# Kernel tuning notes

Hardware: AMD Instinct MI355X
Metric: run time of the kernel (lower is better)

The kernel has to match this reference:

```python
import jax, jax.numpy as jnp
import numpy as np

NUM_CLASSES = 81
SCORE_THRESH = 0.05
BBOX_XFORM_CLIP = float(np.log(1000.0 / 16.0))
WX, WY, WW, WH = 10.0, 10.0, 5.0, 5.0           # post-processor box_coder weights


def setup_inputs() -> dict:
    key = jax.random.key(0)
    ks = jax.random.split(key, 10)
    R, C, P, H = 2000, 256, 7, 1024
    D = C * P * P  # 12544
    x = jax.random.normal(ks[0], (R, C, P, P), jnp.float32)
    xy = jax.random.uniform(ks[1], (R, 2), jnp.float32) * 600.0
    wh = jax.random.uniform(ks[2], (R, 2), jnp.float32) * 200.0 + 1.0
    boxes = jnp.concatenate([xy, xy + wh], axis=1)  # valid xyxy proposals
    s = 0.01
    W6 = jax.random.normal(ks[3], (D, H), jnp.float32) * s
    b6 = jnp.zeros((H,), jnp.float32)
    W7 = jax.random.normal(ks[4], (H, H), jnp.float32) * s
    b7 = jnp.zeros((H,), jnp.float32)
    Wcls = jax.random.normal(ks[5], (H, NUM_CLASSES), jnp.float32) * s
    bcls = jnp.zeros((NUM_CLASSES,), jnp.float32)
    Wbox = jax.random.normal(ks[6], (H, NUM_CLASSES * 4), jnp.float32) * s
    bbox_b = jnp.zeros((NUM_CLASSES * 4,), jnp.float32)
    return {"x": x, "boxes": boxes, "W6": W6, "b6": b6, "W7": W7, "b7": b7,
            "Wcls": Wcls, "bcls": bcls, "Wbox": Wbox, "bbox_b": bbox_b}


def _decode(reg, boxes):
    w = boxes[:, 2] - boxes[:, 0] + 1.0
    h = boxes[:, 3] - boxes[:, 1] + 1.0
    cx = boxes[:, 0] + 0.5 * w
    cy = boxes[:, 1] + 0.5 * h
    dx = reg[..., 0] / WX
    dy = reg[..., 1] / WY
    dw = jnp.minimum(reg[..., 2] / WW, BBOX_XFORM_CLIP)
    dh = jnp.minimum(reg[..., 3] / WH, BBOX_XFORM_CLIP)
    pcx = dx * w[:, None] + cx[:, None]
    pcy = dy * h[:, None] + cy[:, None]
    pw = jnp.exp(dw) * w[:, None]
    ph = jnp.exp(dh) * h[:, None]
    return jnp.stack([pcx - 0.5 * pw, pcy - 0.5 * ph,
                      pcx + 0.5 * pw - 1.0, pcy + 0.5 * ph - 1.0], axis=-1)


def reference(x, boxes, W6, b6, W7, b7, Wcls, bcls, Wbox, bbox_b):
    R = x.shape[0]
    f = x.reshape(R, -1)                          # [R, 12544]
    f6 = jax.nn.relu(f @ W6 + b6)                 # roi_output, [R, 1024]
    f7 = jax.nn.relu(f6 @ W7 + b7)                # [R, 1024]
    probs = jax.nn.softmax(f7 @ Wcls + bcls, axis=-1)       # [R, 81]
    reg = (f7 @ Wbox + bbox_b).reshape(R, NUM_CLASSES, 4)   # [R, 81, 4]
    dec = _decode(reg, boxes)                     # [R, 81, 4]
    # per_class_extend, fixed-shape: drop background class 0, mask below threshold
    pj = probs[:, 1:]                             # [R, 80]
    bj = dec[:, 1:, :]                            # [R, 80, 4]
    keep = pj > SCORE_THRESH
    scores_m = jnp.where(keep, pj, 0.0)
    boxes_m = jnp.where(keep[..., None], bj, 0.0).reshape(R, -1)  # [R, 320]
    return jnp.concatenate([scores_m, boxes_m, f6], axis=-1)      # [R, 1424]
```

## Files before the change

kernel.cpp:

```cpp
#include <hip/hip_runtime.h>
#include <stdint.h>

typedef float f32x4 __attribute__((ext_vector_type(4)));
typedef __bf16 bf16x8 __attribute__((ext_vector_type(8)));
typedef unsigned short us4 __attribute__((ext_vector_type(4)));

__device__ __forceinline__ unsigned short f32_to_bf16(float f) {
  union { float f; uint32_t u; } v; v.f = f;
  return (unsigned short)((v.u + 0x7FFFu + ((v.u >> 16) & 1u)) >> 16);
}

__device__ __forceinline__ void gload16(const void* g, void* l) {
  __builtin_amdgcn_global_load_lds((const __attribute__((address_space(1))) void*)g,
                                   (__attribute__((address_space(3))) void*)l, 16, 0, 0);
}

template <int EPI>
__global__ __launch_bounds__(256, 2) void gemm_bf16(
    const unsigned short* __restrict__ A, const unsigned short* __restrict__ Bt,
    int M, int NB, int K, int Mtiles, int Ntiles, int splits,
    float* __restrict__ outF, unsigned short* __restrict__ outH,
    const float* __restrict__ bias, const float* __restrict__ bias2,
    int NV, size_t splitStride)
{
  __shared__ unsigned short lds[16384];
  const int tid = threadIdx.x;
  const int lane = tid & 63;
  const int wave = tid >> 6;

  int bid = blockIdx.x;
  const int mt = bid % Mtiles; bid /= Mtiles;
  const int nt = bid % Ntiles; bid /= Ntiles;
  const int sp = bid;

  const int nK = K >> 5;
  const int chunk = nK / splits;
  const int kBegin = sp * chunk;
  const int kEnd = kBegin + chunk;

  const int rowl = tid & 127;
  const int k8l = tid >> 7;
  int aRow = mt * 128 + rowl; if (aRow > M - 1) aRow = M - 1;
  int bRow = nt * 128 + rowl; if (bRow > NB - 1) bRow = NB - 1;
  const unsigned short* gA = A + (size_t)aRow * K + k8l * 8;
  const unsigned short* gB = Bt + (size_t)bRow * K + k8l * 8;

  const int k8 = lane >> 4;
  const int rsel = lane & 15;
  const int wrBase = (wave >> 1) * 64;
  const int wcBase = (wave & 1) * 64;
  int aOff[4], bOff[4];
#pragma unroll
  for (int m = 0; m < 4; ++m) aOff[m] = (k8 * 128 + wrBase + m * 16 + rsel) * 8;
#pragma unroll
  for (int n = 0; n < 4; ++n) bOff[n] = 4096 + (k8 * 128 + wcBase + n * 16 + rsel) * 8;

  f32x4 acc[4][4];
  const f32x4 zero = {0.f, 0.f, 0.f, 0.f};
#pragma unroll
  for (int m = 0; m < 4; ++m)
#pragma unroll
    for (int n = 0; n < 4; ++n) acc[m][n] = zero;

  auto stage = [&](int kt, int b) {
    const unsigned short* a = gA + kt * 32;
    const unsigned short* bsrc = gB + kt * 32;
    unsigned short* base = &lds[b * 8192];
    gload16(a,         base + tid * 8);
    gload16(a + 16,    base + (tid + 256) * 8);
    gload16(bsrc,      base + 4096 + tid * 8);
    gload16(bsrc + 16, base + 4096 + (tid + 256) * 8);
  };

  stage(kBegin, 0);
  __syncthreads();
  int cur = 0;
  for (int kt = kBegin; kt < kEnd; ++kt) {
    if (kt + 1 < kEnd) stage(kt + 1, cur ^ 1);
    const int cbase = cur * 8192;
    bf16x8 af[4], bfv[4];
#pragma unroll
    for (int m = 0; m < 4; ++m) af[m] = *(const bf16x8*)&lds[cbase + aOff[m]];
#pragma unroll
    for (int n = 0; n < 4; ++n) bfv[n] = *(const bf16x8*)&lds[cbase + bOff[n]];
#pragma unroll
    for (int m = 0; m < 4; ++m)
#pragma unroll
      for (int n = 0; n < 4; ++n)
        acc[m][n] = __builtin_amdgcn_mfma_f32_16x16x32_bf16(af[m], bfv[n], acc[m][n], 0, 0, 0);
    __syncthreads();
    cur ^= 1;
  }

  const int colBase = nt * 128 + wcBase + rsel;
  const int rowBase = mt * 128 + wrBase + (lane >> 4) * 4;
#pragma unroll
  for (int m = 0; m < 4; ++m) {
#pragma unroll
    for (int n = 0; n < 4; ++n) {
      const int col = colBase + n * 16;
#pragma unroll
      for (int j = 0; j < 4; ++j) {
        const int row = rowBase + m * 16 + j;
        if (row < M) {
          float v = acc[m][n][j];
          if (EPI == 0) {
            outF[sp * splitStride + (size_t)row * 1024 + col] = v;
          } else if (EPI == 1) {
            v += bias[col];
            v = fmaxf(v, 0.f);
            outH[(size_t)row * 1024 + col] = f32_to_bf16(v);
          } else {
            if (col < NV) {
              v += (col < 81) ? bias[col] : bias2[col - 81];
              outF[(size_t)row * NV + col] = v;
            }
          }
        }
      }
    }
  }
}

__global__ void transpose_to_bf16(const float* __restrict__ src, unsigned short* __restrict__ dst,
                                  int R, int C, int dstRowOff, int dstLd) {
  __shared__ unsigned short tile[64][66];
  const int c0 = blockIdx.x * 64, r0 = blockIdx.y * 64;
  const int t = threadIdx.x;
  const bool fast = ((C & 3) == 0) && (c0 + 64 <= C);
  const int lr0 = t >> 4;
  const int lc4 = (t & 15) * 4;
#pragma unroll
  for (int i = 0; i < 4; ++i) {
    const int lr = lr0 + i * 16;
    const size_t rowOff = (size_t)(r0 + lr) * C;
    if (fast) {
      f32x4 v = *(const f32x4*)(src + rowOff + c0 + lc4);
#pragma unroll
      for (int j = 0; j < 4; ++j) tile[lr][lc4 + j] = f32_to_bf16(v[j]);
    } else {
#pragma unroll
      for (int j = 0; j < 4; ++j) {
        const int c = c0 + lc4 + j;
        tile[lr][lc4 + j] = (c < C) ? f32_to_bf16(src[rowOff + c]) : (unsigned short)0;
      }
    }
  }
  __syncthreads();
  const int kk = (t & 15) * 4;
#pragma unroll
  for (int i = 0; i < 4; ++i) {
    const int lc = lr0 + i * 16;
    const int c = c0 + lc;
    if (c < C) {
      us4 h;
#pragma unroll
      for (int j = 0; j < 4; ++j) h[j] = tile[kk + j][lc];
      *(us4*)(dst + (size_t)(dstRowOff + c) * dstLd + r0 + kk) = h;
    }
  }
}

__global__ void convert_to_bf16(const float* __restrict__ src, unsigned short* __restrict__ dst,
                                long n4) {
  for (long i = blockIdx.x * (long)blockDim.x + threadIdx.x; i < n4;
       i += (long)gridDim.x * blockDim.x) {
    f32x4 v = *(const f32x4*)(src + i * 4);
    us4 h;
#pragma unroll
    for (int j = 0; j < 4; ++j) h[j] = f32_to_bf16(v[j]);
    *(us4*)(dst + i * 4) = h;
  }
}

__global__ void reduce_bias_relu(const float* __restrict__ Cp, int splits, size_t sstride,
                                 const float* __restrict__ b6, float* __restrict__ out,
                                 unsigned short* __restrict__ f6b, int M) {
  const long total = (long)M * 256;
  for (long i = blockIdx.x * (long)blockDim.x + threadIdx.x; i < total;
       i += (long)gridDim.x * blockDim.x) {
    const long row = i >> 8;
    const int c4 = (int)(i & 255) * 4;
    const size_t off = ((size_t)row << 10) + c4;
    f32x4 s = *(const f32x4*)(Cp + off);
    for (int sp = 1; sp < splits; ++sp) s += *(const f32x4*)(Cp + (size_t)sp * sstride + off);
    s += *(const f32x4*)(b6 + c4);
    us4 h;
#pragma unroll
    for (int j = 0; j < 4; ++j) { s[j] = fmaxf(s[j], 0.f); h[j] = f32_to_bf16(s[j]); }
    *(f32x4*)(out + (size_t)row * 1424 + 400 + c4) = s;
    *(us4*)(f6b + off) = h;
  }
}

__global__ void head_epilogue(const float* __restrict__ cb, const float* __restrict__ boxes,
                              float* __restrict__ out, int M) {
  const float CLIP = 4.135166556742356f;
  const int row = blockIdx.x * 4 + (threadIdx.x >> 6);
  const int lane = threadIdx.x & 63;
  if (row >= M) return;
  const float* L = cb + (size_t)row * 405;
  const float v0 = L[lane];
  const float v1 = (lane < 17) ? L[64 + lane] : -1e30f;
  float mx = fmaxf(v0, v1);
#pragma unroll
  for (int off = 32; off; off >>= 1) mx = fmaxf(mx, __shfl_xor(mx, off, 64));
  float e0 = __expf(v0 - mx);
  float e1 = (lane < 17) ? __expf(v1 - mx) : 0.f;
  float sum = e0 + e1;
#pragma unroll
  for (int off = 32; off; off >>= 1) sum += __shfl_xor(sum, off, 64);
  const float inv = 1.f / sum;

  const float bx0 = boxes[row * 4 + 0], by0 = boxes[row * 4 + 1];
  const float bx1 = boxes[row * 4 + 2], by1 = boxes[row * 4 + 3];
  const float w = bx1 - bx0 + 1.f, h = by1 - by0 + 1.f;
  const float cx = bx0 + 0.5f * w, cy = by0 + 0.5f * h;
  float* orow = out + (size_t)row * 1424;

#pragma unroll
  for (int t = 0; t < 2; ++t) {
    const int c = (t == 0) ? lane : 64 + lane;
    const bool valid = (t == 0) ? (lane >= 1) : (lane < 17);
    if (valid) {
      const float p = ((t == 0) ? e0 : e1) * inv;
      const float* rg = L + 81 + c * 4;
      const float dx = rg[0] * 0.1f, dy = rg[1] * 0.1f;
      const float dw = fminf(rg[2] * 0.2f, CLIP), dh = fminf(rg[3] * 0.2f, CLIP);
      const float pcx = dx * w + cx, pcy = dy * h + cy;
      const float pw = __expf(dw) * w, ph = __expf(dh) * h;
      const bool keep = p > 0.05f;
      orow[c - 1] = keep ? p : 0.f;
      float* ob = orow + 80 + (c - 1) * 4;
      ob[0] = keep ? (pcx - 0.5f * pw) : 0.f;
      ob[1] = keep ? (pcy - 0.5f * ph) : 0.f;
      ob[2] = keep ? (pcx + 0.5f * pw - 1.f) : 0.f;
      ob[3] = keep ? (pcy + 0.5f * ph - 1.f) : 0.f;
    }
  }
}

extern "C" void kernel_launch(void* const* d_in, const int* in_sizes, int n_in,
                              void* d_out, int out_size, void* d_ws, size_t ws_size,
                              hipStream_t stream) {
  const float* x     = (const float*)d_in[0];
  const float* boxes = (const float*)d_in[1];
  const float* W6    = (const float*)d_in[2];
  const float* b6    = (const float*)d_in[3];
  const float* W7    = (const float*)d_in[4];
  const float* b7    = (const float*)d_in[5];
  const float* Wcls  = (const float*)d_in[6];
  const float* bcls  = (const float*)d_in[7];
  const float* Wbox  = (const float*)d_in[8];
  const float* bboxb = (const float*)d_in[9];
  float* out = (float*)d_out;

  const int M = 2000, D = 12544, H = 1024;
  char* p = (char*)d_ws;
  auto carve = [&](size_t bytes) { char* r = p; p += (bytes + 255) & ~(size_t)255; return r; };
  unsigned short* xb   = (unsigned short*)carve((size_t)M * D * 2);
  unsigned short* W6T  = (unsigned short*)carve((size_t)H * D * 2);
  unsigned short* W7T  = (unsigned short*)carve((size_t)H * H * 2);
  unsigned short* WcbT = (unsigned short*)carve((size_t)405 * H * 2);
  unsigned short* f6b  = (unsigned short*)carve((size_t)M * H * 2);
  unsigned short* f7b  = (unsigned short*)carve((size_t)M * H * 2);
  float* cbv           = (float*)carve((size_t)M * 405 * 4);
  size_t used = (size_t)(p - (char*)d_ws);
  int splits = 8;
  while (splits > 1 && used + (size_t)splits * M * H * 4 + 1024 > ws_size) splits >>= 1;
  float* Cp = (float*)carve((size_t)splits * M * H * 4);

  convert_to_bf16<<<4096, 256, 0, stream>>>(x, xb, (long)M * D / 4);
  transpose_to_bf16<<<dim3(16, 196), 256, 0, stream>>>(W6, W6T, D, H, 0, D);
  transpose_to_bf16<<<dim3(16, 16), 256, 0, stream>>>(W7, W7T, H, H, 0, H);
  transpose_to_bf16<<<dim3(2, 16), 256, 0, stream>>>(Wcls, WcbT, H, 81, 0, H);
  transpose_to_bf16<<<dim3(6, 16), 256, 0, stream>>>(Wbox, WcbT, H, 324, 81, H);

  gemm_bf16<0><<<16 * 8 * splits, 256, 0, stream>>>(xb, W6T, M, H, D, 16, 8, splits,
                                                    Cp, nullptr, nullptr, nullptr, 0,
                                                    (size_t)M * H);
  reduce_bias_relu<<<2048, 256, 0, stream>>>(Cp, splits, (size_t)M * H, b6, out, f6b, M);

  gemm_bf16<1><<<16 * 8, 256, 0, stream>>>(f6b, W7T, M, H, H, 16, 8, 1,
                                           nullptr, f7b, b7, nullptr, 0, 0);

  gemm_bf16<2><<<16 * 4, 256, 0, stream>>>(f7b, WcbT, M, 405, H, 16, 4, 1,
                                           cbv, nullptr, bcls, bboxb, 405, 0);

  head_epilogue<<<(M + 3) / 4, 256, 0, stream>>>(cbv, boxes, out, M);
}
```

Before: 424.7 us.

## Remap GEMM workgroups across XCDs and split-K the second FC layer

```diff
diff --git a/kernel.cpp b/kernel.cpp
--- a/kernel.cpp
+++ b/kernel.cpp
@@ -28,10 +28,12 @@
   const int lane = tid & 63;
   const int wave = tid >> 6;
 
-  int bid = blockIdx.x;
-  const int mt = bid % Mtiles; bid /= Mtiles;
-  const int nt = bid % Ntiles; bid /= Ntiles;
-  const int sp = bid;
+  const int nwg = Mtiles * Ntiles * splits;
+  const int per = nwg >> 3;
+  int wg = (blockIdx.x & 7) * per + (blockIdx.x >> 3);
+  const int nt = wg % Ntiles; wg /= Ntiles;
+  const int mt = wg % Mtiles; wg /= Mtiles;
+  const int sp = wg;
 
   const int nK = K >> 5;
   const int chunk = nK / splits;
@@ -173,9 +175,9 @@
   }
 }
 
-__global__ void reduce_bias_relu(const float* __restrict__ Cp, int splits, size_t sstride,
-                                 const float* __restrict__ b6, float* __restrict__ out,
-                                 unsigned short* __restrict__ f6b, int M) {
+__global__ void reduce_bias_act(const float* __restrict__ Cp, int splits, size_t sstride,
+                                const float* __restrict__ bias, float* __restrict__ outF32,
+                                unsigned short* __restrict__ outBf, int M) {
   const long total = (long)M * 256;
   for (long i = blockIdx.x * (long)blockDim.x + threadIdx.x; i < total;
        i += (long)gridDim.x * blockDim.x) {
@@ -184,12 +186,12 @@
     const size_t off = ((size_t)row << 10) + c4;
     f32x4 s = *(const f32x4*)(Cp + off);
     for (int sp = 1; sp < splits; ++sp) s += *(const f32x4*)(Cp + (size_t)sp * sstride + off);
-    s += *(const f32x4*)(b6 + c4);
+    s += *(const f32x4*)(bias + c4);
     us4 h;
 #pragma unroll
     for (int j = 0; j < 4; ++j) { s[j] = fmaxf(s[j], 0.f); h[j] = f32_to_bf16(s[j]); }
-    *(f32x4*)(out + (size_t)row * 1424 + 400 + c4) = s;
-    *(us4*)(f6b + off) = h;
+    if (outF32) *(f32x4*)(outF32 + (size_t)row * 1424 + 400 + c4) = s;
+    *(us4*)(outBf + off) = h;
   }
 }
 
@@ -279,10 +281,18 @@
   gemm_bf16<0><<<16 * 8 * splits, 256, 0, stream>>>(xb, W6T, M, H, D, 16, 8, splits,
                                                     Cp, nullptr, nullptr, nullptr, 0,
                                                     (size_t)M * H);
-  reduce_bias_relu<<<2048, 256, 0, stream>>>(Cp, splits, (size_t)M * H, b6, out, f6b, M);
-
-  gemm_bf16<1><<<16 * 8, 256, 0, stream>>>(f6b, W7T, M, H, H, 16, 8, 1,
-                                           nullptr, f7b, b7, nullptr, 0, 0);
+  reduce_bias_act<<<2048, 256, 0, stream>>>(Cp, splits, (size_t)M * H, b6, out, f6b, M);
+
+  const int splits2 = (splits >= 2) ? 2 : 1;
+  if (splits2 == 2) {
+    gemm_bf16<0><<<16 * 8 * 2, 256, 0, stream>>>(f6b, W7T, M, H, H, 16, 8, 2,
+                                                 Cp, nullptr, nullptr, nullptr, 0,
+                                                 (size_t)M * H);
+    reduce_bias_act<<<2048, 256, 0, stream>>>(Cp, 2, (size_t)M * H, b7, nullptr, f7b, M);
+  } else {
+    gemm_bf16<1><<<16 * 8, 256, 0, stream>>>(f6b, W7T, M, H, H, 16, 8, 1,
+                                             nullptr, f7b, b7, nullptr, 0, 0);
+  }
 
   gemm_bf16<2><<<16 * 4, 256, 0, stream>>>(f7b, WcbT, M, 405, H, 16, 4, 1,
                                            cbv, nullptr, bcls, bboxb, 405, 0);
```

After: 407.3 us. 1.04x faster.
